# Kernel optimization log

Measured on AMD Instinct MI355X. Metric: run time of the kernel, lower is better.

## Reference

```python
import jax, jax.numpy as jnp
import numpy as np

B, N, DIM = 1, 1024, 2048
HEADS, KV_HEADS, DH = 16, 2, 128
GQ = HEADS // KV_HEADS
CMP_BLK, CMP_STRIDE = 32, 16
SEL_BLK, N_SEL = 64, 4
WIN = 128
MEM_KV = 1
SCALE = DH ** -0.5
NEG = -1e10


def rmsnorm(x, g):
    return x * jax.lax.rsqrt(jnp.mean(x * x, axis=-1, keepdims=True) + 1e-6) * g


def rope(x):
    # interleaved rotary (rotary-embedding-torch convention), theta=10000
    n, d = x.shape[-2], x.shape[-1]
    inv = 1.0 / (10000.0 ** (jnp.arange(0, d, 2, dtype=jnp.float32) / d))
    ang = jnp.arange(n, dtype=jnp.float32)[:, None] * inv  # (n, d/2)
    cos, sin = jnp.cos(ang), jnp.sin(ang)
    x1, x2 = x[..., 0::2], x[..., 1::2]
    return jnp.stack([x1 * cos - x2 * sin, x1 * sin + x2 * cos], axis=-1).reshape(x.shape)


def _gqa_attend(q, k, v):
    # q: (B, HEADS, N, DH); k, v: (B, KV_HEADS, J, DH). heads split h-major into (kv_h, gq).
    qg = q.reshape(B, KV_HEADS, GQ, N, DH)
    sim = jnp.einsum('bhgnd,bhjd->bhgnj', qg, k) * SCALE
    attn = jax.nn.softmax(sim, axis=-1)
    out = jnp.einsum('bhgnj,bhjd->bhgnd', attn, v)
    return out.reshape(B, HEADS, N, DH), sim


def _fwd(x, g_norm, W_qkv, k_pos, v_pos, mem_kv, Wk1, bk1, Wk2, bk2, Wv1, bv1, Wv2, bv2, Wg, bg, W_out):
    dim_inner = HEADS * DH
    dim_kv = KV_HEADS * DH
    xn = rmsnorm(x, g_norm)
    qkv = xn @ W_qkv
    q, k, v = jnp.split(qkv, [dim_inner, dim_inner + dim_kv], axis=-1)
    q = q.reshape(B, N, HEADS, DH).transpose(0, 2, 1, 3)
    k = k.reshape(B, N, KV_HEADS, DH).transpose(0, 2, 1, 3)
    v = v.reshape(B, N, KV_HEADS, DH).transpose(0, 2, 1, 3)

    # ---- compressed branch (pre-rotary q/k): overlapping windows -> MLP per block ----
    ov = CMP_BLK - CMP_STRIDE
    n_win = N // CMP_STRIDE
    widx = jnp.arange(n_win)[:, None] * CMP_STRIDE + jnp.arange(CMP_BLK)[None, :]
    kp = jnp.pad(k, ((0, 0), (0, 0), (ov, 0), (0, 0)))
    vp = jnp.pad(v, ((0, 0), (0, 0), (ov, 0), (0, 0)))
    kwin = kp[:, :, widx, :] + k_pos[None, :, None]  # (B,KV,n_win,CMP_BLK,DH)
    vwin = vp[:, :, widx, :] + v_pos[None, :, None]

    def mlp(w, W1, b1, W2, b2):
        f = w.reshape(B, KV_HEADS, n_win, CMP_BLK * DH)
        return jax.nn.relu(f @ W1 + b1) @ W2 + b2

    ck = mlp(kwin, Wk1, bk1, Wk2, bk2)
    cv = mlp(vwin, Wv1, bv1, Wv2, bv2)
    ck = jnp.concatenate([jnp.broadcast_to(mem_kv[0][None], (B, KV_HEADS, MEM_KV, DH)), ck], axis=2)
    cv = jnp.concatenate([jnp.broadcast_to(mem_kv[1][None], (B, KV_HEADS, MEM_KV, DH)), cv], axis=2)
    cmp_out, csim = _gqa_attend(q, ck, cv)

    # ---- rotary embeddings for fine + sliding branches ----
    q = rope(q)
    k = rope(k)

    # ---- top-k block selection from compressed similarities ----
    n_fine = N // SEL_BLK
    cpf = SEL_BLK // CMP_STRIDE
    imp = csim[..., MEM_KV:].mean(axis=2)  # (B,KV,N,n_win): mean over grouped queries
    imp = imp.reshape(B, KV_HEADS, N, n_fine, cpf).mean(axis=-1)
    qi = jnp.arange(N) // SEL_BLK
    diag = qi[:, None] == jnp.arange(n_fine)[None, :]
    imp = jnp.where(diag, NEG, imp)  # own block masked out of scoring
    imp = jax.nn.softmax(jnp.pad(imp, ((0, 0), (0, 0), (0, 0), (1, 0)), constant_values=-1000.0), axis=-1)[..., 1:]
    _, sel = jax.lax.top_k(imp, N_SEL)  # (B,KV,N,N_SEL)
    own = jnp.broadcast_to(qi[None, None, :, None], (B, KV_HEADS, N, 1))
    sel = jnp.concatenate([sel, own], axis=-1)  # always attend the query's own block

    # ---- fine (selected-block) attention ----
    kb = k.reshape(B, KV_HEADS, n_fine, SEL_BLK, DH)
    vb = v.reshape(B, KV_HEADS, n_fine, SEL_BLK, DH)
    gather = jax.vmap(jax.vmap(lambda blocks, idx: blocks[idx]))  # over B, KV_HEADS
    t_tot = (N_SEL + 1) * SEL_BLK
    fk = gather(kb, sel).reshape(B, KV_HEADS, N, t_tot, DH)
    fv = gather(vb, sel).reshape(B, KV_HEADS, N, t_tot, DH)
    qg = q.reshape(B, KV_HEADS, GQ, N, DH)
    fsim = jnp.einsum('bhgnd,bhntd->bhgnt', qg, fk) * SCALE
    fattn = jax.nn.softmax(fsim, axis=-1)
    fine_out = jnp.einsum('bhgnt,bhntd->bhgnd', fattn, fv).reshape(B, HEADS, N, DH)

    # ---- sliding window attention (non-causal, exact windowsize) ----
    kf = jnp.repeat(k, GQ, axis=1)
    vf = jnp.repeat(v, GQ, axis=1)
    nb = N // WIN
    qb = q.reshape(B, HEADS, nb, WIN, DH)
    kpad = jnp.pad(kf, ((0, 0), (0, 0), (WIN, WIN), (0, 0))).reshape(B, HEADS, nb + 2, WIN, DH)
    vpad = jnp.pad(vf, ((0, 0), (0, 0), (WIN, WIN), (0, 0))).reshape(B, HEADS, nb + 2, WIN, DH)
    kwin3 = jnp.concatenate([kpad[:, :, i:i + nb] for i in range(3)], axis=3)  # (B,H,nb,3W,DH)
    vwin3 = jnp.concatenate([vpad[:, :, i:i + nb] for i in range(3)], axis=3)
    qoff = jnp.arange(WIN)
    koff = jnp.arange(3 * WIN) - WIN
    rel_ok = jnp.abs(qoff[:, None] - koff[None, :]) <= WIN  # (W, 3W)
    kglob = jnp.arange(nb)[:, None] * WIN + koff[None, :]
    in_range = (kglob >= 0) & (kglob < N)  # (nb, 3W)
    mask = rel_ok[None, :, :] & in_range[:, None, :]  # (nb, W, 3W)
    ssim = jnp.einsum('bhnid,bhnjd->bhnij', qb, kwin3) * SCALE
    ssim = jnp.where(mask, ssim, NEG)
    sattn = jax.nn.softmax(ssim, axis=-1)
    slide_out = jnp.einsum('bhnij,bhnjd->bhnid', sattn, vwin3).reshape(B, HEADS, N, DH)

    # ---- learned sigmoid gate combine: (compressed, fine, sliding) ----
    gates = jax.nn.sigmoid(xn @ Wg + bg).reshape(B, N, HEADS, 3).transpose(0, 2, 1, 3)
    out = cmp_out * gates[..., 0:1] + fine_out * gates[..., 1:2] + slide_out * gates[..., 2:3]
    out = out.transpose(0, 2, 1, 3).reshape(B, N, HEADS * DH)
    return out @ W_out


def setup_inputs():
    key = jax.random.key(0)
    ks = jax.random.split(key, 12)
    s = 0.02
    dim_inner, dim_kv, cdim = HEADS * DH, KV_HEADS * DH, CMP_BLK * DH
    rn = lambda k, shape: jax.random.normal(k, shape, jnp.float32) * s
    return {
        'x': jax.random.normal(ks[0], (B, N, DIM), jnp.float32),
        'g_norm': jnp.ones((DIM,), jnp.float32),
        'W_qkv': rn(ks[1], (DIM, dim_inner + 2 * dim_kv)),
        'k_pos': rn(ks[2], (KV_HEADS, CMP_BLK, DH)),
        'v_pos': rn(ks[3], (KV_HEADS, CMP_BLK, DH)),
        'mem_kv': rn(ks[4], (2, KV_HEADS, MEM_KV, DH)),
        'Wk1': rn(ks[5], (cdim, cdim)), 'bk1': jnp.zeros((cdim,), jnp.float32),
        'Wk2': rn(ks[6], (cdim, DH)), 'bk2': jnp.zeros((DH,), jnp.float32),
        'Wv1': rn(ks[7], (cdim, cdim)), 'bv1': jnp.zeros((cdim,), jnp.float32),
        'Wv2': rn(ks[8], (cdim, DH)), 'bv2': jnp.zeros((DH,), jnp.float32),
        'Wg': rn(ks[9], (DIM, 3 * HEADS)),
        'bg': jnp.tile(jnp.array([-2.0, -2.0, 2.0], jnp.float32), HEADS),
        'W_out': rn(ks[10], (dim_inner, DIM)),
    }


def reference(x, g_norm, W_qkv, k_pos, v_pos, mem_kv, Wk1, bk1, Wk2, bk2, Wv1, bv1, Wv2, bv2, Wg, bg, W_out):
    return _fwd(x, g_norm, W_qkv, k_pos, v_pos, mem_kv, Wk1, bk1, Wk2, bk2, Wv1, bv1, Wv2, bv2, Wg, bg, W_out)
```

## Files before the change

### kernel.cpp

```cpp
#include <hip/hip_runtime.h>
#include <hip/hip_bf16.h>
#include <math.h>

typedef __hip_bfloat16 bf16;
typedef __attribute__((ext_vector_type(8))) short bf16x8;
typedef __attribute__((ext_vector_type(4))) float f32x4;

#define N_TOK 1024
#define DIM 2048
#define NHEADS 16
#define KVH 2
#define DH 128
#define GQ 8
#define NWIN 64
#define CMP_BLK 32
#define NCMP 65
#define NFINE 16
#define SEL_BLK 64
#define T_TOT 320
#define CDIM 4096
#define SCALE 0.08838834764831845f

static __device__ __forceinline__ float b2f(bf16 v){ return __bfloat162float(v); }
static __device__ __forceinline__ float bfbits2f(unsigned int u){
  union { unsigned int i; float f; } x; x.i = u << 16; return x.f;
}
static __device__ __forceinline__ unsigned short f2bf(float f){
  union { float f; unsigned u; } x; x.f = f;
  unsigned r = x.u + 0x7fffu + ((x.u >> 16) & 1u);
  return (unsigned short)(r >> 16);
}

__global__ __launch_bounds__(256) void rmsnorm_kernel(const float* __restrict__ x,
                                                      const float* __restrict__ g,
                                                      float* __restrict__ xn,
                                                      unsigned short* __restrict__ xnh,
                                                      unsigned short* __restrict__ xnl){
  int n = blockIdx.x, tid = threadIdx.x;
  __shared__ float red[256];
  const float* row = x + (size_t)n*DIM;
  float vals[8];
  float s = 0.f;
  #pragma unroll
  for (int i = 0; i < 8; ++i){ float v = row[tid + i*256]; vals[i] = v; s += v*v; }
  red[tid] = s; __syncthreads();
  for (int st = 128; st > 0; st >>= 1){ if (tid < st) red[tid] += red[tid+st]; __syncthreads(); }
  float scale = 1.0f / sqrtf(red[0]/(float)DIM + 1e-6f);
  #pragma unroll
  for (int i = 0; i < 8; ++i){
    int c = tid + i*256;
    float v = vals[i]*scale*g[c];
    xn[(size_t)n*DIM + c] = v;
    unsigned short h = f2bf(v);
    int sl = c >> 5, kk = c & 31;
    size_t o = (size_t)sl*(N_TOK*32) + (size_t)n*32 + kk;
    xnh[o] = h;
    xnl[o] = f2bf(v - bfbits2f(h));
  }
}

__global__ __launch_bounds__(256) void transpose_split_kernel(const float* __restrict__ W, int ldw,
                                                              int ncols,
                                                              unsigned short* __restrict__ Th,
                                                              unsigned short* __restrict__ Tl){
  __shared__ float t[64][65];
  int bx = blockIdx.x;
  int by = blockIdx.y;
  int tid = threadIdx.x;
  #pragma unroll
  for (int i = 0; i < 16; ++i){
    int idx = tid + i*256;
    int r = idx >> 6, c = idx & 63;
    t[r][c] = W[(size_t)(by*64 + r)*ldw + bx*64 + c];
  }
  __syncthreads();
  #pragma unroll
  for (int i = 0; i < 16; ++i){
    int idx = tid + i*256;
    int nl = idx >> 6, kl = idx & 63;
    float v = t[kl][nl];
    unsigned short h = f2bf(v);
    unsigned short l = f2bf(v - bfbits2f(h));
    int s = by*2 + (kl >> 5), kk = kl & 31;
    size_t o = (size_t)s*((size_t)ncols*32) + (size_t)(bx*64 + nl)*32 + kk;
    Th[o] = h;
    Tl[o] = l;
  }
}

__global__ __launch_bounds__(256) void gemm_splitk_kernel(const void* __restrict__ Av, int a_is_bf16,
                                                          const float* __restrict__ afold,
                                                          const float* __restrict__ B, int ldb,
                                                          float* __restrict__ C,
                                                          int M, int N, int K, int kchunk){
  __shared__ __align__(16) float As[16*68];
  __shared__ __align__(16) float Bs[16*68];
  int tid = threadIdx.x;
  int tx = tid & 15, ty = tid >> 4;
  int m0 = blockIdx.y * 64, n0 = blockIdx.x * 64;
  int kz = blockIdx.z * kchunk;
  const float* Af = (const float*)Av;
  const bf16*  Ab = (const bf16*)Av;
  float c[4][4] = {};
  for (int k0 = kz; k0 < kz + kchunk; k0 += 16){
    #pragma unroll
    for (int i = 0; i < 4; ++i){
      int idx = tid + i*256;
      int kk = idx & 15, m = idx >> 4;
      size_t aidx = (size_t)(m0+m)*K + k0 + kk;
      float av = a_is_bf16 ? b2f(Ab[aidx]) : Af[aidx];
      if (afold) av = fmaxf(av + afold[k0+kk], 0.f);
      As[kk*68 + m] = av;
    }
    #pragma unroll
    for (int i = 0; i < 4; ++i){
      int idx = tid + i*256;
      int nn = idx & 63, kk = idx >> 6;
      int col = n0 + nn;
      Bs[kk*68 + nn] = (col < N) ? B[(size_t)(k0+kk)*ldb + col] : 0.f;
    }
    __syncthreads();
    #pragma unroll
    for (int kk = 0; kk < 16; ++kk){
      float a[4], b[4];
      *(float4*)a = *(const float4*)&As[kk*68 + ty*4];
      *(float4*)b = *(const float4*)&Bs[kk*68 + tx*4];
      #pragma unroll
      for (int i = 0; i < 4; ++i)
        #pragma unroll
        for (int j = 0; j < 4; ++j)
          c[i][j] += a[i]*b[j];
    }
    __syncthreads();
  }
  #pragma unroll
  for (int i = 0; i < 4; ++i){
    int row = m0 + ty*4 + i;
    #pragma unroll
    for (int j = 0; j < 4; ++j){
      int col = n0 + tx*4 + j;
      if (col < N) atomicAdd(&C[(size_t)row*N + col], c[i][j]);
    }
  }
}

__global__ __launch_bounds__(256) void gemm_mlp2_fused_kernel(const float* __restrict__ hbuf2,
    const float* __restrict__ bk1, const float* __restrict__ bv1,
    const float* __restrict__ Wk2, const float* __restrict__ Wv2,
    float* __restrict__ ckb, float* __restrict__ cvb){
  const int kvsel = blockIdx.z >> 5;
  const int kz = (blockIdx.z & 31) * 128;
  const float* Af    = hbuf2 + (size_t)kvsel*128*CDIM;
  const float* afold = kvsel ? bv1 : bk1;
  const float* B     = kvsel ? Wv2 : Wk2;
  float* C           = kvsel ? cvb : ckb;
  __shared__ __align__(16) float As[16*68];
  __shared__ __align__(16) float Bs[16*68];
  int tid = threadIdx.x;
  int tx = tid & 15, ty = tid >> 4;
  int m0 = blockIdx.y * 64, n0 = blockIdx.x * 64;
  float c[4][4] = {};
  for (int k0 = kz; k0 < kz + 128; k0 += 16){
    #pragma unroll
    for (int i = 0; i < 4; ++i){
      int idx = tid + i*256;
      int kk = idx & 15, m = idx >> 4;
      float av = Af[(size_t)(m0+m)*CDIM + k0 + kk];
      av = fmaxf(av + afold[k0+kk], 0.f);
      As[kk*68 + m] = av;
    }
    #pragma unroll
    for (int i = 0; i < 4; ++i){
      int idx = tid + i*256;
      int nn = idx & 63, kk = idx >> 6;
      Bs[kk*68 + nn] = B[(size_t)(k0+kk)*DH + n0 + nn];
    }
    __syncthreads();
    #pragma unroll
    for (int kk = 0; kk < 16; ++kk){
      float a[4], b[4];
      *(float4*)a = *(const float4*)&As[kk*68 + ty*4];
      *(float4*)b = *(const float4*)&Bs[kk*68 + tx*4];
      #pragma unroll
      for (int i = 0; i < 4; ++i)
        #pragma unroll
        for (int j = 0; j < 4; ++j)
          c[i][j] += a[i]*b[j];
    }
    __syncthreads();
  }
  #pragma unroll
  for (int i = 0; i < 4; ++i){
    int row = m0 + ty*4 + i;
    #pragma unroll
    for (int j = 0; j < 4; ++j){
      int col = n0 + tx*4 + j;
      atomicAdd(&C[(size_t)row*DH + col], c[i][j]);
    }
  }
}

__global__ __launch_bounds__(256) void gemm_mfma_mlp1_kernel(const unsigned short* __restrict__ fh,
                                                             const unsigned short* __restrict__ fl,
                                                             const float* __restrict__ Wk1,
                                                             const float* __restrict__ Wv1,
                                                             float* __restrict__ hbuf2){
  const int kvsel = blockIdx.z >> 3;
  const int slab0 = (blockIdx.z & 7) * 16;
  const int kz = slab0 * 32;
  const unsigned short* Ah = fh + (size_t)kvsel*524288 + (size_t)slab0*4096;
  const unsigned short* Al = fl + (size_t)kvsel*524288 + (size_t)slab0*4096;
  const float* B = kvsel ? Wv1 : Wk1;
  float* C = hbuf2 + (size_t)kvsel*524288;
  const int n0 = blockIdx.x * 64;
  const int m0 = blockIdx.y * 64;
  const int tid = threadIdx.x;
  const int wid = tid >> 6, lane = tid & 63;
  const int l15 = lane & 15, lg = lane >> 4;
  const int colL = wid*16 + l15;
  __shared__ __align__(16) float Bs[2][32][68];

  f32x4 acc[4];
  #pragma unroll
  for (int m = 0; m < 4; ++m) acc[m] = (f32x4){0.f,0.f,0.f,0.f};

  const unsigned short* ahp[4];
  const unsigned short* alp[4];
  #pragma unroll
  for (int m = 0; m < 4; ++m){
    size_t ro = (size_t)(m0 + m*16 + l15)*32 + lg*8;
    ahp[m] = Ah + ro;
    alp[m] = Al + ro;
  }
  const int sr = tid >> 3, sc = (tid & 7) * 8;

  float4 rb0, rb1;
  int4 rah[4], ral[4];
  {
    const float* bp = B + (size_t)(kz + sr)*CDIM + n0 + sc;
    rb0 = *(const float4*)(bp);
    rb1 = *(const float4*)(bp + 4);
    #pragma unroll
    for (int m = 0; m < 4; ++m){
      rah[m] = *(const int4*)(ahp[m]);
      ral[m] = *(const int4*)(alp[m]);
    }
  }

  #pragma unroll 1
  for (int s = 0; s < 16; ++s){
    const int buf = s & 1;
    *(float4*)&Bs[buf][sr][sc]     = rb0;
    *(float4*)&Bs[buf][sr][sc + 4] = rb1;
    int4 cah[4], cal[4];
    #pragma unroll
    for (int m = 0; m < 4; ++m){ cah[m] = rah[m]; cal[m] = ral[m]; }
    __syncthreads();
    if (s + 1 < 16){
      const int kr = kz + (s+1)*32;
      const float* bp = B + (size_t)(kr + sr)*CDIM + n0 + sc;
      rb0 = *(const float4*)(bp);
      rb1 = *(const float4*)(bp + 4);
      #pragma unroll
      for (int m = 0; m < 4; ++m){
        rah[m] = *(const int4*)(ahp[m] + (size_t)(s+1)*4096);
        ral[m] = *(const int4*)(alp[m] + (size_t)(s+1)*4096);
      }
    }
    float bv[8];
    #pragma unroll
    for (int j = 0; j < 8; ++j) bv[j] = Bs[buf][lg*8 + j][colL];
    bf16x8 bh, bl;
    #pragma unroll
    for (int j = 0; j < 8; ++j){
      unsigned short h = f2bf(bv[j]);
      bh[j] = (short)h;
      bl[j] = (short)f2bf(bv[j] - bfbits2f(h));
    }
    #pragma unroll
    for (int m = 0; m < 4; ++m){
      union { int4 i; bf16x8 v; } uah, ual;
      uah.i = cah[m]; ual.i = cal[m];
      acc[m] = __builtin_amdgcn_mfma_f32_16x16x32_bf16(uah.v, bh, acc[m], 0, 0, 0);
      acc[m] = __builtin_amdgcn_mfma_f32_16x16x32_bf16(ual.v, bh, acc[m], 0, 0, 0);
      acc[m] = __builtin_amdgcn_mfma_f32_16x16x32_bf16(uah.v, bl, acc[m], 0, 0, 0);
    }
  }
  const int col = n0 + colL;
  #pragma unroll
  for (int m = 0; m < 4; ++m)
    #pragma unroll
    for (int r = 0; r < 4; ++r){
      const int row = m0 + m*16 + lg*4 + r;
      atomicAdd(&C[(size_t)row*CDIM + col], acc[m][r]);
    }
}

#define QKV_MFMA1(ACC, AH, AL, BH, BL) do{ \
    union { int4 i; bf16x8 v; } ubh_, ubl_; \
    ubh_.i = BH; ubl_.i = BL; \
    _Pragma("unroll") \
    for (int m_ = 0; m_ < 2; ++m_){ \
      union { int4 i; bf16x8 v; } uah_, ual_; \
      uah_.i = AH[m_]; ual_.i = AL[m_]; \
      ACC[m_] = __builtin_amdgcn_mfma_f32_16x16x32_bf16(uah_.v, ubh_.v, ACC[m_], 0, 0, 0); \
      ACC[m_] = __builtin_amdgcn_mfma_f32_16x16x32_bf16(ual_.v, ubh_.v, ACC[m_], 0, 0, 0); \
      ACC[m_] = __builtin_amdgcn_mfma_f32_16x16x32_bf16(uah_.v, ubl_.v, ACC[m_], 0, 0, 0); \
    } \
  }while(0)
#define QKV_FILL(AH, AL, BH0, BL0, BH1, BL1, S) do{ \
    _Pragma("unroll") \
    for (int m_ = 0; m_ < 2; ++m_){ \
      AH[m_] = *(const int4*)(aph[m_] + (size_t)(S)*ASTR); \
      AL[m_] = *(const int4*)(apl[m_] + (size_t)(S)*ASTR); \
    } \
    BH0 = *(const int4*)(bph0 + (size_t)(S)*BSTR); \
    BL0 = *(const int4*)(bpl0 + (size_t)(S)*BSTR); \
    BH1 = *(const int4*)(bph1 + (size_t)(S)*BSTR); \
    BL1 = *(const int4*)(bpl1 + (size_t)(S)*BSTR); \
  }while(0)

__global__ __launch_bounds__(256) void gemm_mfma_qkvT_kernel(const unsigned short* __restrict__ Ah,
                                                             const unsigned short* __restrict__ Al,
                                                             const unsigned short* __restrict__ BhT,
                                                             const unsigned short* __restrict__ BlT,
                                                             float* __restrict__ Cq,
                                                             float* __restrict__ Ckv){
  const int n0 = blockIdx.x * 128;
  const int m0 = blockIdx.y * 32;
  const int tid = threadIdx.x;
  const int wid = tid >> 6, lane = tid & 63;
  const int l15 = lane & 15, lg = lane >> 4;
  const int col0 = n0 + wid*32 + l15;
  const int col1 = col0 + 16;
  const size_t ASTR = (size_t)N_TOK*32;
  const size_t BSTR = (size_t)2560*32;

  f32x4 acc0[2], acc1[2];
  #pragma unroll
  for (int m = 0; m < 2; ++m){ acc0[m] = (f32x4){0.f,0.f,0.f,0.f}; acc1[m] = (f32x4){0.f,0.f,0.f,0.f}; }

  const unsigned short* aph[2];
  const unsigned short* apl[2];
  #pragma unroll
  for (int m = 0; m < 2; ++m){
    size_t ro = (size_t)(m0 + m*16 + l15)*32 + lg*8;
    aph[m] = Ah + ro;
    apl[m] = Al + ro;
  }
  const unsigned short* bph0 = BhT + (size_t)col0*32 + lg*8;
  const unsigned short* bpl0 = BlT + (size_t)col0*32 + lg*8;
  const unsigned short* bph1 = BhT + (size_t)col1*32 + lg*8;
  const unsigned short* bpl1 = BlT + (size_t)col1*32 + lg*8;

  int4 r0ah[2], r0al[2], r1ah[2], r1al[2];
  int4 r0bh0, r0bl0, r0bh1, r0bl1, r1bh0, r1bl0, r1bh1, r1bl1;
  QKV_FILL(r0ah, r0al, r0bh0, r0bl0, r0bh1, r0bl1, 0);
  QKV_FILL(r1ah, r1al, r1bh0, r1bl0, r1bh1, r1bl1, 1);

  #pragma unroll 1
  for (int s = 0; s < 64; s += 2){
    QKV_MFMA1(acc0, r0ah, r0al, r0bh0, r0bl0);
    QKV_MFMA1(acc1, r0ah, r0al, r0bh1, r0bl1);
    if (s + 2 < 64) QKV_FILL(r0ah, r0al, r0bh0, r0bl0, r0bh1, r0bl1, s+2);
    QKV_MFMA1(acc0, r1ah, r1al, r1bh0, r1bl0);
    QKV_MFMA1(acc1, r1ah, r1al, r1bh1, r1bl1);
    if (s + 3 < 64) QKV_FILL(r1ah, r1al, r1bh0, r1bl0, r1bh1, r1bl1, s+3);
  }
  #pragma unroll
  for (int m = 0; m < 2; ++m)
    #pragma unroll
    for (int r = 0; r < 4; ++r){
      const int row = m0 + m*16 + lg*4 + r;
      if (col0 < 2048) Cq[(size_t)row*DIM + col0] = acc0[m][r];
      else             Ckv[(size_t)row*512 + (col0 - 2048)] = acc0[m][r];
      if (col1 < 2048) Cq[(size_t)row*DIM + col1] = acc1[m][r];
      else             Ckv[(size_t)row*512 + (col1 - 2048)] = acc1[m][r];
    }
}

#define OUT_MFMA1(ACC, AA, BH, BL) do{ \
    union { int4 i; bf16x8 v; } ubh_, ubl_; \
    ubh_.i = BH; ubl_.i = BL; \
    _Pragma("unroll") \
    for (int m_ = 0; m_ < 2; ++m_){ \
      union { int4 i; bf16x8 v; } ua_; ua_.i = AA[m_]; \
      ACC[m_] = __builtin_amdgcn_mfma_f32_16x16x32_bf16(ua_.v, ubh_.v, ACC[m_], 0, 0, 0); \
      ACC[m_] = __builtin_amdgcn_mfma_f32_16x16x32_bf16(ua_.v, ubl_.v, ACC[m_], 0, 0, 0); \
    } \
  }while(0)
#define OUT_FILL(AA, BH0, BL0, BH1, BL1, S) do{ \
    _Pragma("unroll") \
    for (int m_ = 0; m_ < 2; ++m_) \
      AA[m_] = *(const int4*)(ap[m_] + (size_t)(S)*ASTR); \
    BH0 = *(const int4*)(bph0 + (size_t)(S)*BSTR); \
    BL0 = *(const int4*)(bpl0 + (size_t)(S)*BSTR); \
    BH1 = *(const int4*)(bph1 + (size_t)(S)*BSTR); \
    BL1 = *(const int4*)(bpl1 + (size_t)(S)*BSTR); \
  }while(0)

__global__ __launch_bounds__(256) void gemm_mfma_outT_kernel(const unsigned short* __restrict__ AT,
                                                             const unsigned short* __restrict__ BhT,
                                                             const unsigned short* __restrict__ BlT,
                                                             float* __restrict__ C){
  const int n0 = blockIdx.x * 128;
  const int m0 = blockIdx.y * 32;
  const int tid = threadIdx.x;
  const int wid = tid >> 6, lane = tid & 63;
  const int l15 = lane & 15, lg = lane >> 4;
  const int col0 = n0 + wid*32 + l15;
  const int col1 = col0 + 16;
  const size_t ASTR = (size_t)N_TOK*32;
  const size_t BSTR = (size_t)2048*32;

  f32x4 acc0[2], acc1[2];
  #pragma unroll
  for (int m = 0; m < 2; ++m){ acc0[m] = (f32x4){0.f,0.f,0.f,0.f}; acc1[m] = (f32x4){0.f,0.f,0.f,0.f}; }

  const unsigned short* ap[2];
  #pragma unroll
  for (int m = 0; m < 2; ++m)
    ap[m] = AT + (size_t)(m0 + m*16 + l15)*32 + lg*8;
  const unsigned short* bph0 = BhT + (size_t)col0*32 + lg*8;
  const unsigned short* bpl0 = BlT + (size_t)col0*32 + lg*8;
  const unsigned short* bph1 = BhT + (size_t)col1*32 + lg*8;
  const unsigned short* bpl1 = BlT + (size_t)col1*32 + lg*8;

  int4 r0a[2], r1a[2];
  int4 r0bh0, r0bl0, r0bh1, r0bl1, r1bh0, r1bl0, r1bh1, r1bl1;
  OUT_FILL(r0a, r0bh0, r0bl0, r0bh1, r0bl1, 0);
  OUT_FILL(r1a, r1bh0, r1bl0, r1bh1, r1bl1, 1);

  #pragma unroll 1
  for (int s = 0; s < 64; s += 2){
    OUT_MFMA1(acc0, r0a, r0bh0, r0bl0);
    OUT_MFMA1(acc1, r0a, r0bh1, r0bl1);
    if (s + 2 < 64) OUT_FILL(r0a, r0bh0, r0bl0, r0bh1, r0bl1, s+2);
    OUT_MFMA1(acc0, r1a, r1bh0, r1bl0);
    OUT_MFMA1(acc1, r1a, r1bh1, r1bl1);
    if (s + 3 < 64) OUT_FILL(r1a, r1bh0, r1bl0, r1bh1, r1bl1, s+3);
  }
  #pragma unroll
  for (int m = 0; m < 2; ++m)
    #pragma unroll
    for (int r = 0; r < 4; ++r){
      const int row = m0 + m*16 + lg*4 + r;
      C[(size_t)row*DIM + col0] = acc0[m][r];
      C[(size_t)row*DIM + col1] = acc1[m][r];
    }
}

__global__ __launch_bounds__(256) void rope_kernel(const float* __restrict__ q,
    const float* __restrict__ kv, bf16* __restrict__ qr, bf16* __restrict__ kr){
  int n = blockIdx.x, tid = threadIdx.x;
  const float* qrow = q + (size_t)n*DIM;
  bf16* qrrow = qr + (size_t)n*DIM;
  #pragma unroll
  for (int i = 0; i < 4; ++i){
    int p = tid + i*256;
    int hd = p >> 6, ii = p & 63;
    float inv = powf(10000.f, -(float)ii/64.f);
    float ang = (float)n * inv;
    float cs = cosf(ang), sn = sinf(ang);
    float x1 = qrow[hd*DH + 2*ii], x2 = qrow[hd*DH + 2*ii + 1];
    qrrow[hd*DH + 2*ii]     = __float2bfloat16(x1*cs - x2*sn);
    qrrow[hd*DH + 2*ii + 1] = __float2bfloat16(x1*sn + x2*cs);
  }
  if (tid < 128){
    int h = tid >> 6, ii = tid & 63;
    float inv = powf(10000.f, -(float)ii/64.f);
    float ang = (float)n * inv;
    float cs = cosf(ang), sn = sinf(ang);
    const float* kvrow = kv + (size_t)n*512;
    float x1 = kvrow[h*DH + 2*ii], x2 = kvrow[h*DH + 2*ii + 1];
    bf16* krrow = kr + (size_t)n*256;
    krrow[h*DH + 2*ii]     = __float2bfloat16(x1*cs - x2*sn);
    krrow[h*DH + 2*ii + 1] = __float2bfloat16(x1*sn + x2*cs);
  }
}

__global__ __launch_bounds__(256) void build_f_kernel(const float* __restrict__ kv,
    const float* __restrict__ k_pos, const float* __restrict__ v_pos,
    unsigned short* __restrict__ fh, unsigned short* __restrict__ fl){
  int bw2 = blockIdx.x;
  int kvsel = bw2 >> 7, bw = bw2 & 127;
  int voff = kvsel * 256;
  const float* pos = kvsel ? v_pos : k_pos;
  int h = bw >> 6, w = bw & 63;
  int tid = threadIdx.x;
  for (int idx = tid; idx < CMP_BLK*DH; idx += 256){
    int j = idx >> 7, d = idx & 127;
    int t = w*16 + j - 16;
    float kvv = (t >= 0) ? kv[(size_t)t*512 + voff + h*DH + d] : 0.f;
    float v = kvv + pos[(h*CMP_BLK + j)*DH + d];
    unsigned short hh = f2bf(v);
    int sl = idx >> 5, kk = idx & 31;
    size_t o = (size_t)kvsel*524288 + (size_t)sl*4096 + (size_t)bw*32 + kk;
    fh[o] = hh;
    fl[o] = f2bf(v - bfbits2f(hh));
  }
}

__global__ __launch_bounds__(256) void assemble_kernel(const float* __restrict__ ckb,
    const float* __restrict__ cvb, const float* __restrict__ mem_kv,
    const float* __restrict__ bk2, const float* __restrict__ bv2,
    float* __restrict__ ck, float* __restrict__ cv){
  int j = blockIdx.x;
  int tid = threadIdx.x;
  int h = tid >> 7, d = tid & 127;
  float kvx, vvx;
  if (j == 0){
    kvx = mem_kv[(0*KVH + h)*DH + d];
    vvx = mem_kv[(1*KVH + h)*DH + d];
  } else {
    kvx = ckb[((size_t)h*NWIN + (j-1))*DH + d] + bk2[d];
    vvx = cvb[((size_t)h*NWIN + (j-1))*DH + d] + bv2[d];
  }
  ck[((size_t)h*NCMP + j)*DH + d] = kvx;
  cv[((size_t)h*NCMP + j)*DH + d] = vvx;
}

__global__ __launch_bounds__(256) void cmp_attn_kernel(const float* __restrict__ q,
    const float* __restrict__ ck, const float* __restrict__ cv,
    bf16* __restrict__ cmp_o, int* __restrict__ sel){
  int bx = blockIdx.x;
  int h = bx >> 10, n = bx & 1023;
  int tid = threadIdx.x;
  __shared__ float cks[NCMP*129];
  __shared__ float qs[GQ*DH];
  __shared__ float sims[GQ*66];
  __shared__ float red[GQ*32];
  __shared__ float impb[NFINE];
  for (int idx = tid; idx < NCMP*DH; idx += 256){
    int j = idx >> 7, d = idx & 127;
    cks[j*129 + d] = ck[((size_t)h*NCMP + j)*DH + d];
  }
  for (int idx = tid; idx < GQ*DH; idx += 256)
    qs[idx] = q[(size_t)n*DIM + h*(GQ*DH) + idx];
  __syncthreads();
  for (int p = tid; p < GQ*NCMP; p += 256){
    int g = p / NCMP, j = p % NCMP;
    float acc = 0.f;
    const float* qp = &qs[g*DH];
    const float* kp = &cks[j*129];
    #pragma unroll 4
    for (int d = 0; d < DH; ++d) acc += qp[d]*kp[d];
    sims[g*66 + j] = acc * SCALE;
  }
  __syncthreads();
  if (tid < NFINE){
    float s = 0.f;
    for (int g = 0; g < GQ; ++g)
      #pragma unroll
      for (int c = 0; c < 4; ++c)
        s += sims[g*66 + 1 + tid*4 + c];
    impb[tid] = s;
  }
  __syncthreads();
  if (tid == 0){
    int own = n >> 6;
    impb[own] = -1e30f;
    int selbuf[5];
    #pragma unroll
    for (int r = 0; r < 4; ++r){
      float best = -1e38f; int bi = 0;
      for (int f = 0; f < NFINE; ++f)
        if (impb[f] > best){ best = impb[f]; bi = f; }
      selbuf[r] = bi; impb[bi] = -1e38f;
    }
    selbuf[4] = own;
    for (int r = 0; r < 5; ++r) sel[(size_t)(h*N_TOK + n)*8 + r] = selbuf[r];
  }
  int g = tid >> 5, lane = tid & 31;
  float m = -1e38f;
  for (int j = lane; j < NCMP; j += 32) m = fmaxf(m, sims[g*66 + j]);
  red[g*32 + lane] = m; __syncthreads();
  for (int st = 16; st > 0; st >>= 1){ if (lane < st) red[g*32+lane] = fmaxf(red[g*32+lane], red[g*32+lane+st]); __syncthreads(); }
  float gm = red[g*32]; __syncthreads();
  float ps = 0.f;
  for (int j = lane; j < NCMP; j += 32){ float e = expf(sims[g*66+j] - gm); sims[g*66+j] = e; ps += e; }
  red[g*32+lane] = ps; __syncthreads();
  for (int st = 16; st > 0; st >>= 1){ if (lane < st) red[g*32+lane] += red[g*32+lane+st]; __syncthreads(); }
  float inv = 1.f / red[g*32]; __syncthreads();
  for (int j = lane; j < NCMP; j += 32) sims[g*66+j] *= inv;
  __syncthreads();
  for (int p = tid; p < GQ*DH; p += 256){
    int gg = p >> 7, d = p & 127;
    float acc = 0.f;
    const float* cvp = cv + (size_t)h*NCMP*DH + d;
    for (int j = 0; j < NCMP; ++j) acc += sims[gg*66 + j] * cvp[j*DH];
    cmp_o[(size_t)n*DIM + (h*GQ + gg)*DH + d] = __float2bfloat16(acc);
  }
}

#define FA_LOADK(blk) do{ \
    const bf16* p_ = kr + (size_t)((blk)*SEL_BLK + tK)*256 + h*DH; \
    k0 = *(const int4*)(p_ + dK);      \
    k1 = *(const int4*)(p_ + dK + 32); \
    k2 = *(const int4*)(p_ + dK + 64); \
    k3 = *(const int4*)(p_ + dK + 96); \
  }while(0)
#define FA_STOREK1(reg, db) do{ \
    unsigned w0_=(unsigned)(reg).x, w1_=(unsigned)(reg).y, w2_=(unsigned)(reg).z, w3_=(unsigned)(reg).w; \
    float* d_ = &kvbuf[(size_t)(db)*66 + tK]; \
    d_[0]   = bfbits2f(w0_ & 0xffffu); d_[66]  = bfbits2f(w0_ >> 16); \
    d_[132] = bfbits2f(w1_ & 0xffffu); d_[198] = bfbits2f(w1_ >> 16); \
    d_[264] = bfbits2f(w2_ & 0xffffu); d_[330] = bfbits2f(w2_ >> 16); \
    d_[396] = bfbits2f(w3_ & 0xffffu); d_[462] = bfbits2f(w3_ >> 16); \
  }while(0)
#define FA_STOREK do{ FA_STOREK1(k0,(dK)); FA_STOREK1(k1,(dK+32)); FA_STOREK1(k2,(dK+64)); FA_STOREK1(k3,(dK+96)); }while(0)
#define FA_QK(tile) do{ \
    float acc0_ = 0.f, acc1_ = 0.f; \
    const float* qp_ = &qs[qi*DH]; \
    const float* kp_ = &kvbuf[2*tx]; \
    _Pragma("unroll") \
    for (int d_ = 0; d_ < DH; d_ += 4){ \
      float4 a_ = *(const float4*)(qp_ + d_); \
      float2 b0_ = *(const float2*)(kp_ + (size_t)(d_  )*66); \
      float2 b1_ = *(const float2*)(kp_ + (size_t)(d_+1)*66); \
      float2 b2_ = *(const float2*)(kp_ + (size_t)(d_+2)*66); \
      float2 b3_ = *(const float2*)(kp_ + (size_t)(d_+3)*66); \
      acc0_ += a_.x*b0_.x; acc1_ += a_.x*b0_.y; \
      acc0_ += a_.y*b1_.x; acc1_ += a_.y*b1_.y; \
      acc0_ += a_.z*b2_.x; acc1_ += a_.z*b2_.y; \
      acc0_ += a_.w*b3_.x; acc1_ += a_.w*b3_.y; \
    } \
    *(float2*)&sims[(size_t)qi*322 + (tile)*SEL_BLK + 2*tx] = make_float2(acc0_*SCALE, acc1_*SCALE); \
  }while(0)
#define FA_LOADV(blk) do{ \
    const float* p_ = kv + (size_t)((blk)*SEL_BLK + tV)*512 + 256 + h*DH; \
    v0 = *(const float4*)(p_ + dV);         \
    v1 = *(const float4*)(p_ + 4096 + dV);  \
    v2 = *(const float4*)(p_ + 8192 + dV);  \
    v3 = *(const float4*)(p_ + 12288 + dV); \
    v4 = *(const float4*)(p_ + 16384 + dV); \
    v5 = *(const float4*)(p_ + 20480 + dV); \
    v6 = *(const float4*)(p_ + 24576 + dV); \
    v7 = *(const float4*)(p_ + 28672 + dV); \
  }while(0)
#define FA_STOREV do{ \
    float* d_ = &kvbuf[(size_t)tV*132 + dV]; \
    *(float4*)(d_)        = v0; \
    *(float4*)(d_ + 1056) = v1; \
    *(float4*)(d_ + 2112) = v2; \
    *(float4*)(d_ + 3168) = v3; \
    *(float4*)(d_ + 4224) = v4; \
    *(float4*)(d_ + 5280) = v5; \
    *(float4*)(d_ + 6336) = v6; \
    *(float4*)(d_ + 7392) = v7; \
  }while(0)
#define FA_PV(tile) do{ \
    const float* sp_ = &sims[(size_t)qi*322 + (tile)*SEL_BLK]; \
    const float* vp_ = &kvbuf[tx << 2]; \
    _Pragma("unroll 8") \
    for (int t_ = 0; t_ < SEL_BLK; ++t_){ \
      float p_ = sp_[t_]; \
      float4 vv_ = *(const float4*)(vp_ + (size_t)t_*132); \
      av0 += p_*vv_.x; av1 += p_*vv_.y; av2 += p_*vv_.z; av3 += p_*vv_.w; \
    } \
  }while(0)

__global__ __launch_bounds__(256) void fine_attn_kernel(const bf16* __restrict__ qr,
    const bf16* __restrict__ kr, const float* __restrict__ kv,
    const int* __restrict__ sel, bf16* __restrict__ fine_o){
  int bx = blockIdx.x;
  int h = bx >> 10, n = bx & 1023;
  int tid = threadIdx.x;
  __shared__ __align__(16) float kvbuf[8448];
  __shared__ __align__(16) float qs[GQ*DH];
  __shared__ float sims[GQ*322];
  __shared__ float red[GQ*32];
  const int qi = tid >> 5, tx = tid & 31;

  int s0_, s1_, s2_, s3_, s4_;
  {
    const int* sp = sel + (size_t)(h*N_TOK + n)*8;
    int b0 = sp[0], b1 = sp[1], b2 = sp[2], b3 = sp[3], b4 = sp[4];
    s0_ = (b0 < 0) ? 0 : (b0 > 15 ? 15 : b0);
    s1_ = (b1 < 0) ? 0 : (b1 > 15 ? 15 : b1);
    s2_ = (b2 < 0) ? 0 : (b2 > 15 ? 15 : b2);
    s3_ = (b3 < 0) ? 0 : (b3 > 15 ? 15 : b3);
    s4_ = (b4 < 0) ? 0 : (b4 > 15 ? 15 : b4);
  }
  for (int idx = tid; idx < GQ*DH; idx += 256)
    qs[idx] = b2f(qr[(size_t)n*DIM + h*(GQ*DH) + idx]);

  const int tK = tid & 63;
  const int dK = (tid >> 6) << 3;
  int4 k0, k1, k2, k3;
  FA_LOADK(s0_);
  __syncthreads(); FA_STOREK; __syncthreads(); FA_LOADK(s1_); FA_QK(0);
  __syncthreads(); FA_STOREK; __syncthreads(); FA_LOADK(s2_); FA_QK(1);
  __syncthreads(); FA_STOREK; __syncthreads(); FA_LOADK(s3_); FA_QK(2);
  __syncthreads(); FA_STOREK; __syncthreads(); FA_LOADK(s4_); FA_QK(3);
  __syncthreads(); FA_STOREK; __syncthreads();                FA_QK(4);

  const int tV = tid >> 5;
  const int dV = (tid & 31) << 2;
  float4 v0, v1, v2, v3, v4, v5, v6, v7;
  FA_LOADV(s0_);
  __syncthreads();

  {
    int g = qi, lane = tx;
    float m = -1e38f;
    for (int t = lane; t < T_TOT; t += 32) m = fmaxf(m, sims[g*322 + t]);
    red[g*32+lane] = m; __syncthreads();
    for (int st = 16; st > 0; st >>= 1){ if (lane < st) red[g*32+lane] = fmaxf(red[g*32+lane], red[g*32+lane+st]); __syncthreads(); }
    float gm = red[g*32]; __syncthreads();
    float ps = 0.f;
    for (int t = lane; t < T_TOT; t += 32){ float e = expf(sims[g*322+t] - gm); sims[g*322+t] = e; ps += e; }
    red[g*32+lane] = ps; __syncthreads();
    for (int st = 16; st > 0; st >>= 1){ if (lane < st) red[g*32+lane] += red[g*32+lane+st]; __syncthreads(); }
    float inv = 1.f / red[g*32]; __syncthreads();
    for (int t = lane; t < T_TOT; t += 32) sims[g*322+t] *= inv;
  }

  float av0 = 0.f, av1 = 0.f, av2 = 0.f, av3 = 0.f;
  __syncthreads(); FA_STOREV; __syncthreads(); FA_LOADV(s1_); FA_PV(0);
  __syncthreads(); FA_STOREV; __syncthreads(); FA_LOADV(s2_); FA_PV(1);
  __syncthreads(); FA_STOREV; __syncthreads(); FA_LOADV(s3_); FA_PV(2);
  __syncthreads(); FA_STOREV; __syncthreads(); FA_LOADV(s4_); FA_PV(3);
  __syncthreads(); FA_STOREV; __syncthreads();                FA_PV(4);
  {
    bf16 o[4];
    o[0] = __float2bfloat16(av0);
    o[1] = __float2bfloat16(av1);
    o[2] = __float2bfloat16(av2);
    o[3] = __float2bfloat16(av3);
    *(ushort4*)(fine_o + (size_t)n*DIM + (h*GQ + qi)*DH + (tx << 2)) = *(const ushort4*)o;
  }
}

__global__ __launch_bounds__(256) void slide_attn_kernel(const bf16* __restrict__ qr,
    const bf16* __restrict__ kr, const float* __restrict__ kv,
    bf16* __restrict__ slide_o){
  int hq = blockIdx.y;
  int qt = blockIdx.x;
  int h = hq >> 3;
  int n0 = qt * 32;
  int tid = threadIdx.x;
  __shared__ float qT[128*36];
  __shared__ float kvb[128*68];
  __shared__ float stT[64*36];

  const int ty  = tid >> 5;
  const int tx  = tid & 31;
  const int qi0 = ty << 2;

  for (int c = tid; c < 512; c += 256){
    int qi = c & 31, d0 = (c >> 5) << 3;
    int4 w = *(const int4*)(qr + (size_t)(n0+qi)*DIM + hq*DH + d0);
    float* dst = &qT[(size_t)d0*36 + qi];
    unsigned int wv[4] = {(unsigned)w.x,(unsigned)w.y,(unsigned)w.z,(unsigned)w.w};
    #pragma unroll
    for (int m = 0; m < 4; ++m){
      dst[(2*m  )*36] = bfbits2f(wv[m] & 0xffffu);
      dst[(2*m+1)*36] = bfbits2f(wv[m] >> 16);
    }
  }

  float acc[4][4] = {};
  float mrow[4] = {-1e30f,-1e30f,-1e30f,-1e30f};
  float lrow[4] = {0.f,0.f,0.f,0.f};
  float arow[4];
  const int kstart = n0 - 128;

  for (int tile = 0; tile < 5; ++tile){
    const int kbase = kstart + tile*64;
    __syncthreads();
    for (int c = tid; c < 1024; c += 256){
      int t = c & 63, d0 = (c >> 6) << 3;
      int kg = kbase + t;
      int kgc = min(max(kg, 0), N_TOK-1);
      int4 w = *(const int4*)(kr + (size_t)kgc*256 + h*DH + d0);
      float* dst = &kvb[(size_t)d0*68 + t];
      unsigned int wv[4] = {(unsigned)w.x,(unsigned)w.y,(unsigned)w.z,(unsigned)w.w};
      #pragma unroll
      for (int m = 0; m < 4; ++m){
        dst[(2*m  )*68] = bfbits2f(wv[m] & 0xffffu);
        dst[(2*m+1)*68] = bfbits2f(wv[m] >> 16);
      }
    }
    __syncthreads();
    float c0[8] = {};
    {
      const float* aP = qT + qi0;
      const float* bP = kvb + (tx << 1);
      #pragma unroll 4
      for (int d = 0; d < 128; ++d){
        float4 a = *(const float4*)(aP + d*36);
        float2 b = *(const float2*)(bP + d*68);
        c0[0] += a.x*b.x; c0[1] += a.x*b.y;
        c0[2] += a.y*b.x; c0[3] += a.y*b.y;
        c0[4] += a.z*b.x; c0[5] += a.z*b.y;
        c0[6] += a.w*b.x; c0[7] += a.w*b.y;
      }
    }
    const int kg0 = kbase + (tx << 1);
    #pragma unroll
    for (int i = 0; i < 4; ++i){
      int qg = n0 + qi0 + i;
      int d0 = qg - kg0, d1 = d0 - 1;
      bool v0 = (kg0   >= 0) && (kg0   < N_TOK) && (d0 <= 128) && (d0 >= -128);
      bool v1 = (kg0+1 >= 0) && (kg0+1 < N_TOK) && (d1 <= 128) && (d1 >= -128);
      float s0 = v0 ? c0[i*2  ]*SCALE : -1e30f;
      float s1 = v1 ? c0[i*2+1]*SCALE : -1e30f;
      float mi = fmaxf(s0, s1);
      #pragma unroll
      for (int off = 1; off < 32; off <<= 1) mi = fmaxf(mi, __shfl_xor(mi, off));
      float mold = mrow[i];
      float mnew = fmaxf(fmaxf(mold, mi), -1e20f);
      arow[i] = expf(mold - mnew);
      mrow[i] = mnew;
      float e0 = expf(s0 - mnew);
      float e1 = expf(s1 - mnew);
      float ps = e0 + e1;
      #pragma unroll
      for (int off = 1; off < 32; off <<= 1) ps += __shfl_xor(ps, off);
      lrow[i] = lrow[i]*arow[i] + ps;
      stT[(size_t)(2*tx  )*36 + qi0 + i] = e0;
      stT[(size_t)(2*tx+1)*36 + qi0 + i] = e1;
    }
    __syncthreads();
    for (int c = tid; c < 2048; c += 256){
      int t = c >> 5, d0 = (c & 31) << 2;
      int kg = kbase + t;
      int kgc = min(max(kg, 0), N_TOK-1);
      float4 v = *(const float4*)(kv + (size_t)kgc*512 + 256 + h*DH + d0);
      *(float4*)&kvb[(size_t)t*128 + d0] = v;
    }
    __syncthreads();
    #pragma unroll
    for (int i = 0; i < 4; ++i){
      float ar = arow[i];
      acc[i][0] *= ar; acc[i][1] *= ar; acc[i][2] *= ar; acc[i][3] *= ar;
    }
    {
      const float* pP = stT + qi0;
      const float* vP = kvb + (tx << 2);
      #pragma unroll 4
      for (int t = 0; t < 64; ++t){
        float4 p = *(const float4*)(pP + t*36);
        float4 v = *(const float4*)(vP + t*128);
        acc[0][0] += p.x*v.x; acc[0][1] += p.x*v.y; acc[0][2] += p.x*v.z; acc[0][3] += p.x*v.w;
        acc[1][0] += p.y*v.x; acc[1][1] += p.y*v.y; acc[1][2] += p.y*v.z; acc[1][3] += p.y*v.w;
        acc[2][0] += p.z*v.x; acc[2][1] += p.z*v.y; acc[2][2] += p.z*v.z; acc[2][3] += p.z*v.w;
        acc[3][0] += p.w*v.x; acc[3][1] += p.w*v.y; acc[3][2] += p.w*v.z; acc[3][3] += p.w*v.w;
      }
    }
  }
  #pragma unroll
  for (int i = 0; i < 4; ++i){
    int row = n0 + qi0 + i;
    float inv = 1.f / lrow[i];
    bf16 o[4];
    o[0] = __float2bfloat16(acc[i][0]*inv);
    o[1] = __float2bfloat16(acc[i][1]*inv);
    o[2] = __float2bfloat16(acc[i][2]*inv);
    o[3] = __float2bfloat16(acc[i][3]*inv);
    *(ushort4*)(slide_o + (size_t)row*DIM + hq*DH + (tx << 2)) = *(const ushort4*)o;
  }
}

__global__ __launch_bounds__(256) void combine_kernel(const bf16* __restrict__ cmp_o,
    const bf16* __restrict__ fine_o, const bf16* __restrict__ slide_o,
    const float* __restrict__ graw, const float* __restrict__ bg,
    unsigned short* __restrict__ ocombT){
  int n = blockIdx.x, tid = threadIdx.x;
  #pragma unroll
  for (int i = 0; i < 8; ++i){
    int c = tid + i*256;
    int hq = c >> 7;
    float g0 = 1.f/(1.f + expf(-(graw[(size_t)n*48 + hq*3 + 0] + bg[hq*3 + 0])));
    float g1 = 1.f/(1.f + expf(-(graw[(size_t)n*48 + hq*3 + 1] + bg[hq*3 + 1])));
    float g2 = 1.f/(1.f + expf(-(graw[(size_t)n*48 + hq*3 + 2] + bg[hq*3 + 2])));
    size_t idx = (size_t)n*DIM + c;
    float v = b2f(cmp_o[idx])*g0 + b2f(fine_o[idx])*g1 + b2f(slide_o[idx])*g2;
    int sl = c >> 5, kk = c & 31;
    ocombT[(size_t)sl*(N_TOK*32) + (size_t)n*32 + kk] = f2bf(v);
  }
}

extern "C" void kernel_launch(void* const* d_in, const int* in_sizes, int n_in,
                              void* d_out, int out_size, void* d_ws, size_t ws_size,
                              hipStream_t stream)
{
  const float* x      = (const float*)d_in[0];
  const float* g_norm = (const float*)d_in[1];
  const float* W_qkv  = (const float*)d_in[2];
  const float* k_pos  = (const float*)d_in[3];
  const float* v_pos  = (const float*)d_in[4];
  const float* mem_kv = (const float*)d_in[5];
  const float* Wk1    = (const float*)d_in[6];
  const float* bk1    = (const float*)d_in[7];
  const float* Wk2    = (const float*)d_in[8];
  const float* bk2    = (const float*)d_in[9];
  const float* Wv1    = (const float*)d_in[10];
  const float* bv1    = (const float*)d_in[11];
  const float* Wv2    = (const float*)d_in[12];
  const float* bv2    = (const float*)d_in[13];
  const float* Wg     = (const float*)d_in[14];
  const float* bg     = (const float*)d_in[15];
  const float* W_out  = (const float*)d_in[16];
  float* out = (float*)d_out;
  (void)ws_size; (void)in_sizes; (void)n_in; (void)out_size;

  char* base = (char*)d_ws;
  float* q     = (float*)(base + 0);
  float* xn    = (float*)(base + 8388608);
  bf16*  qr    = (bf16*) (base + 8388608);
  bf16*  kr    = (bf16*) (base + 12582912);
  unsigned short* ocombT = (unsigned short*)(base + 8388608);
  float* kv    = (float*)(base + 16777216);
  float* hbuf2 = (float*)(base + 18874368);
  bf16*  cmp_o = (bf16*) (base + 18874368);
  float* ckb   = (float*)(base + 23068672);
  float* cvb   = (float*)(base + 23134208);
  float* ck    = (float*)(base + 23199744);
  float* cv    = (float*)(base + 23266304);
  float* gates = (float*)(base + 23332864);
  int*   sel   = (int*)  (base + 23529472);
  bf16*  fine_o  = (bf16*)(base + 0);
  bf16*  slide_o = (bf16*)(base + 4194304);
  unsigned short* xnh  = (unsigned short*)(base + 25165824);
  unsigned short* xnl  = (unsigned short*)(base + 29360128);
  unsigned short* WqhT = (unsigned short*)(base + 33554432);
  unsigned short* WqlT = (unsigned short*)(base + 44040192);
  unsigned short* WohT = WqhT;
  unsigned short* WolT = WqlT;
  unsigned short* fh   = (unsigned short*)(base + 41943040);
  unsigned short* fl   = (unsigned short*)(base + 52428800);

  hipMemsetAsync(gates, 0, (size_t)N_TOK*48*4,   stream);
  hipMemsetAsync(ckb,   0, (size_t)KVH*NWIN*DH*4, stream);
  hipMemsetAsync(cvb,   0, (size_t)KVH*NWIN*DH*4, stream);
  hipMemsetAsync(hbuf2, 0, (size_t)2*128*CDIM*4,  stream);

  transpose_split_kernel<<<dim3(40, 32), 256, 0, stream>>>(W_qkv, 2560, 2560, WqhT, WqlT);
  rmsnorm_kernel<<<N_TOK, 256, 0, stream>>>(x, g_norm, xn, xnh, xnl);
  gemm_splitk_kernel<<<dim3(1, 16, 16), 256, 0, stream>>>(xn, 0, nullptr, Wg, 48, gates, N_TOK, 48, DIM, 128);
  gemm_mfma_qkvT_kernel<<<dim3(20, 32), 256, 0, stream>>>(xnh, xnl, WqhT, WqlT, q, kv);
  transpose_split_kernel<<<dim3(32, 32), 256, 0, stream>>>(W_out, 2048, 2048, WohT, WolT);
  rope_kernel<<<N_TOK, 256, 0, stream>>>(q, kv, qr, kr);
  build_f_kernel<<<256, 256, 0, stream>>>(kv, k_pos, v_pos, fh, fl);
  gemm_mfma_mlp1_kernel<<<dim3(64, 2, 16), 256, 0, stream>>>(fh, fl, Wk1, Wv1, hbuf2);
  gemm_mlp2_fused_kernel<<<dim3(2, 2, 64), 256, 0, stream>>>(hbuf2, bk1, bv1, Wk2, Wv2, ckb, cvb);
  assemble_kernel<<<NCMP, 256, 0, stream>>>(ckb, cvb, mem_kv, bk2, bv2, ck, cv);
  cmp_attn_kernel<<<KVH*N_TOK, 256, 0, stream>>>(q, ck, cv, cmp_o, sel);
  fine_attn_kernel<<<KVH*N_TOK, 256, 0, stream>>>(qr, kr, kv, sel, fine_o);
  slide_attn_kernel<<<dim3(32, 16), 256, 0, stream>>>(qr, kr, kv, slide_o);
  combine_kernel<<<N_TOK, 256, 0, stream>>>(cmp_o, fine_o, slide_o, gates, bg, ocombT);
  gemm_mfma_outT_kernel<<<dim3(16, 32), 256, 0, stream>>>(ocombT, WohT, WolT, out);
}
```

Before: 697.2 us.

## Prefetch sliding-window K/V tiles into registers and use shuffle softmax reductions

The sliding-window attention kernel now issues global loads for the next K tile and the current V tile into registers before the compute phase that precedes their use, so memory latency overlaps the QK and PV loops instead of sitting in front of them. The compressed-attention softmax replaces shared-memory tree reductions and their many block barriers with warp shuffle reductions. The prefetch holds twelve extra vector registers per thread, which may lower occupancy.

```diff
diff --git a/kernel.cpp b/kernel.cpp
--- a/kernel.cpp
+++ b/kernel.cpp
@@ -529,7 +529,6 @@
   __shared__ float cks[NCMP*129];
   __shared__ float qs[GQ*DH];
   __shared__ float sims[GQ*66];
-  __shared__ float red[GQ*32];
   __shared__ float impb[NFINE];
   for (int idx = tid; idx < NCMP*DH; idx += 256){
     int j = idx >> 7, d = idx & 127;
@@ -574,14 +573,13 @@
   int g = tid >> 5, lane = tid & 31;
   float m = -1e38f;
   for (int j = lane; j < NCMP; j += 32) m = fmaxf(m, sims[g*66 + j]);
-  red[g*32 + lane] = m; __syncthreads();
-  for (int st = 16; st > 0; st >>= 1){ if (lane < st) red[g*32+lane] = fmaxf(red[g*32+lane], red[g*32+lane+st]); __syncthreads(); }
-  float gm = red[g*32]; __syncthreads();
+  #pragma unroll
+  for (int off = 16; off > 0; off >>= 1) m = fmaxf(m, __shfl_xor(m, off));
   float ps = 0.f;
-  for (int j = lane; j < NCMP; j += 32){ float e = expf(sims[g*66+j] - gm); sims[g*66+j] = e; ps += e; }
-  red[g*32+lane] = ps; __syncthreads();
-  for (int st = 16; st > 0; st >>= 1){ if (lane < st) red[g*32+lane] += red[g*32+lane+st]; __syncthreads(); }
-  float inv = 1.f / red[g*32]; __syncthreads();
+  for (int j = lane; j < NCMP; j += 32){ float e = expf(sims[g*66+j] - m); sims[g*66+j] = e; ps += e; }
+  #pragma unroll
+  for (int off = 16; off > 0; off >>= 1) ps += __shfl_xor(ps, off);
+  float inv = 1.f / ps;
   for (int j = lane; j < NCMP; j += 32) sims[g*66+j] *= inv;
   __syncthreads();
   for (int p = tid; p < GQ*DH; p += 256){
@@ -732,6 +730,45 @@
   }
 }
 
+#define SL_LOADK(kbase_) do{ \
+    int kg_ = (kbase_) + tS; \
+    int kgc_ = min(max(kg_, 0), N_TOK-1); \
+    const bf16* p_ = kr + (size_t)kgc_*256 + h*DH; \
+    sk0 = *(const int4*)(p_ + dS);      \
+    sk1 = *(const int4*)(p_ + dS + 32); \
+    sk2 = *(const int4*)(p_ + dS + 64); \
+    sk3 = *(const int4*)(p_ + dS + 96); \
+  }while(0)
+#define SL_STOREK1(reg, db) do{ \
+    unsigned w0_=(unsigned)(reg).x, w1_=(unsigned)(reg).y, w2_=(unsigned)(reg).z, w3_=(unsigned)(reg).w; \
+    float* d_ = &kvb[(size_t)(db)*68 + tS]; \
+    d_[0]   = bfbits2f(w0_ & 0xffffu); d_[68]  = bfbits2f(w0_ >> 16); \
+    d_[136] = bfbits2f(w1_ & 0xffffu); d_[204] = bfbits2f(w1_ >> 16); \
+    d_[272] = bfbits2f(w2_ & 0xffffu); d_[340] = bfbits2f(w2_ >> 16); \
+    d_[408] = bfbits2f(w3_ & 0xffffu); d_[476] = bfbits2f(w3_ >> 16); \
+  }while(0)
+#define SL_STOREK do{ SL_STOREK1(sk0,(dS)); SL_STOREK1(sk1,(dS+32)); SL_STOREK1(sk2,(dS+64)); SL_STOREK1(sk3,(dS+96)); }while(0)
+#define SL_LOADV1(reg, kbase_, i_) do{ \
+    int kg_ = (kbase_) + tV + 8*(i_); \
+    int kgc_ = min(max(kg_, 0), N_TOK-1); \
+    reg = *(const float4*)(kv + (size_t)kgc_*512 + 256 + h*DH + dV); \
+  }while(0)
+#define SL_LOADV(kbase_) do{ \
+    SL_LOADV1(sv0,(kbase_),0); SL_LOADV1(sv1,(kbase_),1); SL_LOADV1(sv2,(kbase_),2); SL_LOADV1(sv3,(kbase_),3); \
+    SL_LOADV1(sv4,(kbase_),4); SL_LOADV1(sv5,(kbase_),5); SL_LOADV1(sv6,(kbase_),6); SL_LOADV1(sv7,(kbase_),7); \
+  }while(0)
+#define SL_STOREV do{ \
+    float* d_ = &kvb[(size_t)tV*128 + dV]; \
+    *(float4*)(d_)        = sv0; \
+    *(float4*)(d_ + 1024) = sv1; \
+    *(float4*)(d_ + 2048) = sv2; \
+    *(float4*)(d_ + 3072) = sv3; \
+    *(float4*)(d_ + 4096) = sv4; \
+    *(float4*)(d_ + 5120) = sv5; \
+    *(float4*)(d_ + 6144) = sv6; \
+    *(float4*)(d_ + 7168) = sv7; \
+  }while(0)
+
 __global__ __launch_bounds__(256) void slide_attn_kernel(const bf16* __restrict__ qr,
     const bf16* __restrict__ kr, const float* __restrict__ kv,
     bf16* __restrict__ slide_o){
@@ -747,6 +784,10 @@
   const int ty  = tid >> 5;
   const int tx  = tid & 31;
   const int qi0 = ty << 2;
+  const int tS  = tid & 63;
+  const int dS  = (tid >> 6) << 3;
+  const int tV  = tid >> 5;
+  const int dV  = (tid & 31) << 2;
 
   for (int c = tid; c < 512; c += 256){
     int qi = c & 31, d0 = (c >> 5) << 3;
@@ -766,23 +807,16 @@
   float arow[4];
   const int kstart = n0 - 128;
 
+  int4 sk0, sk1, sk2, sk3;
+  float4 sv0, sv1, sv2, sv3, sv4, sv5, sv6, sv7;
+  SL_LOADK(kstart);
+
   for (int tile = 0; tile < 5; ++tile){
     const int kbase = kstart + tile*64;
     __syncthreads();
-    for (int c = tid; c < 1024; c += 256){
-      int t = c & 63, d0 = (c >> 6) << 3;
-      int kg = kbase + t;
-      int kgc = min(max(kg, 0), N_TOK-1);
-      int4 w = *(const int4*)(kr + (size_t)kgc*256 + h*DH + d0);
-      float* dst = &kvb[(size_t)d0*68 + t];
-      unsigned int wv[4] = {(unsigned)w.x,(unsigned)w.y,(unsigned)w.z,(unsigned)w.w};
-      #pragma unroll
-      for (int m = 0; m < 4; ++m){
-        dst[(2*m  )*68] = bfbits2f(wv[m] & 0xffffu);
-        dst[(2*m+1)*68] = bfbits2f(wv[m] >> 16);
-      }
-    }
+    SL_STOREK;
     __syncthreads();
+    SL_LOADV(kbase);
     float c0[8] = {};
     {
       const float* aP = qT + qi0;
@@ -823,14 +857,9 @@
       stT[(size_t)(2*tx+1)*36 + qi0 + i] = e1;
     }
     __syncthreads();
-    for (int c = tid; c < 2048; c += 256){
-      int t = c >> 5, d0 = (c & 31) << 2;
-      int kg = kbase + t;
-      int kgc = min(max(kg, 0), N_TOK-1);
-      float4 v = *(const float4*)(kv + (size_t)kgc*512 + 256 + h*DH + d0);
-      *(float4*)&kvb[(size_t)t*128 + d0] = v;
-    }
+    SL_STOREV;
     __syncthreads();
+    if (tile + 1 < 5) SL_LOADK(kbase + 64);
     #pragma unroll
     for (int i = 0; i < 4; ++i){
       float ar = arow[i];
```

Result: no change. 693.5 us (-0.5%).
